# Kernel tuning notes

Measured on AMD Instinct MI355X. Metric: run time of the kernel, lower is better.

## Reference

```python
import jax, jax.numpy as jnp
import numpy as np

N = 50000    # nodes
E = 800000   # edges per block
D = 128      # embed_dim
H = 8        # heads
DH = D // H  # head dim
L = 2        # layers / blocks
IN = 128     # in_feats
P = 8192     # pos/neg pairs
FF = 2 * D   # FFN hidden
NEG_SLOPE = 0.2


def layer_norm(x, g, b, eps=1e-5):
    m = x.mean(-1, keepdims=True)
    v = ((x - m) ** 2).mean(-1, keepdims=True)
    return (x - m) / jnp.sqrt(v + eps) * g + b


def setup_inputs() -> dict:
    key = jax.random.key(0)
    ks = jax.random.split(key, 32)
    f32 = jnp.float32
    def w(k, shape, fan_in):
        return jax.random.normal(k, shape, f32) * (1.0 / np.sqrt(fan_in))
    inp = {
        'x': jax.random.normal(ks[0], (N, IN), f32),
        'src': jax.random.randint(ks[1], (L, E), 0, N),
        'dst': jax.random.randint(ks[2], (L, E), 0, N),
        'pos_src': jax.random.randint(ks[3], (P,), 0, N),
        'pos_dst': jax.random.randint(ks[4], (P,), 0, N),
        'neg_src': jax.random.randint(ks[5], (P,), 0, N),
        'neg_dst': jax.random.randint(ks[6], (P,), 0, N),
        # input projection
        'W_in': w(ks[7], (IN, D), IN), 'b_in': jnp.zeros((D,), f32),
        # per-layer attention weights, stacked over L
        'Wq': w(ks[8], (L, D, D), D), 'bq': jnp.zeros((L, D), f32),
        'Wk': w(ks[9], (L, D, D), D), 'bk': jnp.zeros((L, D), f32),
        'Wv': w(ks[10], (L, D, D), D), 'bv': jnp.zeros((L, D), f32),
        'Wo': w(ks[11], (L, D, D), D), 'bo': jnp.zeros((L, D), f32),
        'ln1_g': jnp.ones((L, D), f32), 'ln1_b': jnp.zeros((L, D), f32),
        'Wf1': w(ks[12], (L, D, FF), D), 'bf1': jnp.zeros((L, FF), f32),
        'Wf2': w(ks[13], (L, FF, D), FF), 'bf2': jnp.zeros((L, D), f32),
        'ln2_g': jnp.ones((L, D), f32), 'ln2_b': jnp.zeros((L, D), f32),
        # predictor MLP: D -> D//2 -> 1
        'Wp1': w(ks[14], (D, D // 2), D), 'bp1': jnp.zeros((D // 2,), f32),
        'Wp2': w(ks[15], (D // 2, 1), D // 2), 'bp2': jnp.zeros((1,), f32),
    }
    return inp


def reference(x, src, dst, pos_src, pos_dst, neg_src, neg_dst,
              W_in, b_in, Wq, bq, Wk, bk, Wv, bv, Wo, bo,
              ln1_g, ln1_b, Wf1, bf1, Wf2, bf2, ln2_g, ln2_b,
              Wp1, bp1, Wp2, bp2):
    scale = 1.0 / np.sqrt(DH)
    h = x @ W_in + b_in  # [N, D] (dropout is identity in eval mode)
    for l in range(L):
        s_l, d_l = src[l], dst[l]
        q = (h @ Wq[l] + bq[l]).reshape(N, H, DH)
        k = (h @ Wk[l] + bk[l]).reshape(N, H, DH)
        v = (h @ Wv[l] + bv[l]).reshape(N, H, DH)
        # per-edge attention scores [E, H]
        sc = jnp.einsum('ehd,ehd->eh', q[d_l], k[s_l]) * scale
        # segment softmax over incoming edges of each dst node
        m = jax.ops.segment_max(sc, d_l, num_segments=N)   # [N, H]
        ex = jnp.exp(sc - m[d_l])
        den = jax.ops.segment_sum(ex, d_l, num_segments=N)  # [N, H]
        alpha = ex / (den[d_l] + 1e-9)
        agg = jax.ops.segment_sum(alpha[..., None] * v[s_l], d_l,
                                  num_segments=N).reshape(N, D)
        h = layer_norm(h + agg @ Wo[l] + bo[l], ln1_g[l], ln1_b[l])
        ff = jax.nn.relu(h @ Wf1[l] + bf1[l]) @ Wf2[l] + bf2[l]
        h = layer_norm(h + ff, ln2_g[l], ln2_b[l])

    def predict(a, b):
        z = h[a] * h[b]  # gather-multiply edge scoring
        z = jax.nn.leaky_relu(z @ Wp1 + bp1, NEG_SLOPE)
        return z @ Wp2 + bp2  # [P, 1]

    pos_score = predict(pos_src, pos_dst)
    neg_score = predict(neg_src, neg_dst)
    return (pos_score, neg_score, h)
```

## Files before the change

kernel.cpp:

```cpp
#include <hip/hip_runtime.h>
#include <hip/hip_bf16.h>
#include <math.h>

#define N_NODES 50000
#define NE      800000
#define D       128
#define H       8
#define DH      16
#define NLAYER  2
#define IN_F    128
#define PP      8192
#define FF      256
#define MPAD    50048
#define CAP     96
#define NBIN    196
#define BCAP    48
#define GCAP    4608
#define CHUNK   2048

typedef short  bf16x8 __attribute__((ext_vector_type(8)));
typedef float  f32x4  __attribute__((ext_vector_type(4)));
typedef __hip_bfloat16 bf16;
typedef unsigned short u16;
typedef unsigned int   u32;

__device__ __forceinline__ float bflo(u32 u) { return __uint_as_float(u << 16); }
__device__ __forceinline__ float bfhi(u32 u) { return __uint_as_float(u & 0xffff0000u); }
__device__ __forceinline__ u16 bfbits(float f) { bf16 t = __float2bfloat16(f); return *(u16*)&t; }

__global__ __launch_bounds__(256) void bin_kernel(
    const int* __restrict__ dst, const int* __restrict__ src,
    u32* __restrict__ gbin, int* __restrict__ gbin_cnt)
{
    __shared__ u32 ent[NBIN * BCAP];
    __shared__ int bcnt[NBIN];
    const int t = threadIdx.x, l = blockIdx.y;
    const int base = blockIdx.x * CHUNK;
    if (t < NBIN) bcnt[t] = 0;
    __syncthreads();
    #pragma unroll
    for (int j = 0; j < CHUNK / 256; j++) {
        int e = base + j * 256 + t;
        if (e < NE) {
            int d = dst[(size_t)l * NE + e];
            int s = src[(size_t)l * NE + e];
            int bin = d >> 8;
            int slot = atomicAdd(&bcnt[bin], 1);
            if (slot < BCAP) ent[bin * BCAP + slot] = ((u32)s << 16) | (u32)(d & 255);
        }
    }
    __syncthreads();
    if (t < NBIN) {
        int c = bcnt[t]; if (c > BCAP) c = BCAP;
        if (c > 0) {
            int gb = atomicAdd(&gbin_cnt[l * NBIN + t], c);
            u32* gp = gbin + ((size_t)l * NBIN + t) * GCAP;
            for (int i = 0; i < c; i++)
                if (gb + i < GCAP) gp[gb + i] = ent[t * BCAP + i];
        }
    }
}

__global__ __launch_bounds__(256) void expand_kernel(
    const u32* __restrict__ gbin, const int* __restrict__ gbin_cnt,
    int* __restrict__ cnt, u16* __restrict__ ssrc)
{
    __shared__ int lcnt[256];
    const int t = threadIdx.x, b = blockIdx.x, l = blockIdx.y;
    lcnt[t] = 0;
    __syncthreads();
    int n = gbin_cnt[l * NBIN + b]; if (n > GCAP) n = GCAP;
    const u32* gp = gbin + ((size_t)l * NBIN + b) * GCAP;
    for (int i = t; i < n; i += 256) {
        u32 u = gp[i];
        int dl = (int)(u & 255);
        int pos = atomicAdd(&lcnt[dl], 1);
        if (pos < CAP) {
            int d = (b << 8) + dl;
            ssrc[((size_t)l * N_NODES + d) * CAP + pos] = (u16)(u >> 16);
        }
    }
    __syncthreads();
    int d = (b << 8) + t;
    if (d < N_NODES) cnt[l * N_NODES + d] = lcnt[t];
}

__global__ void prep_kernel(const float* __restrict__ W_in,
                            const float* __restrict__ Wq, const float* __restrict__ Wk,
                            const float* __restrict__ Wv, const float* __restrict__ Wo,
                            const float* __restrict__ Wf1, const float* __restrict__ Wf2,
                            const float* __restrict__ bq, const float* __restrict__ bk,
                            const float* __restrict__ bv,
                            bf16* __restrict__ win_t, bf16* __restrict__ wqkv_t,
                            bf16* __restrict__ wo_t, bf16* __restrict__ wf1_t,
                            bf16* __restrict__ wf2_t, float* __restrict__ bqkv,
                            int* __restrict__ gbin_cnt)
{
    int id = blockIdx.x * blockDim.x + threadIdx.x;
    if (id < 16384) {
        int n = id >> 7, k = id & 127;
        win_t[id] = __float2bfloat16(W_in[k * 128 + n]);
        return;
    }
    id -= 16384;
    if (id < NLAYER * 49152) {
        int l = id / 49152, j = id % 49152;
        int r = j >> 7, k = j & 127;
        const float* Ws; int col;
        if (r < 128) { Ws = Wq; col = r; }
        else {
            int u = r - 128, hh = u >> 5, w = u & 31;
            if (w < 16) { Ws = Wk; col = hh * 16 + w; }
            else        { Ws = Wv; col = hh * 16 + w - 16; }
        }
        wqkv_t[(size_t)l * 49152 + j] = __float2bfloat16(Ws[(size_t)l * 16384 + k * 128 + col]);
        return;
    }
    id -= NLAYER * 49152;
    if (id < NLAYER * 16384) {
        int l = id / 16384, j = id % 16384;
        int n = j >> 7, k = j & 127;
        wo_t[id] = __float2bfloat16(Wo[(size_t)l * 16384 + k * 128 + n]);
        return;
    }
    id -= NLAYER * 16384;
    if (id < NLAYER * 32768) {
        int l = id / 32768, j = id % 32768;
        int n = j >> 7, k = j & 127;
        wf1_t[id] = __float2bfloat16(Wf1[(size_t)l * 32768 + k * 256 + n]);
        return;
    }
    id -= NLAYER * 32768;
    if (id < NLAYER * 32768) {
        int l = id / 32768, j = id % 32768;
        int n = j >> 8, k = j & 255;
        wf2_t[id] = __float2bfloat16(Wf2[(size_t)l * 32768 + k * 128 + n]);
        return;
    }
    id -= NLAYER * 32768;
    if (id < NLAYER * 384) {
        int l = id / 384, r = id % 384;
        float v;
        if (r < 128) v = bq[l * 128 + r];
        else {
            int u = r - 128, hh = u >> 5, w = u & 31;
            v = (w < 16) ? bk[l * 128 + hh * 16 + w] : bv[l * 128 + hh * 16 + w - 16];
        }
        bqkv[l * 384 + r] = v;
        return;
    }
    id -= NLAYER * 384;
    if (id < 2 * NBIN) gbin_cnt[id] = 0;
}

__global__ __launch_bounds__(256) void gemm_in(
    const float* __restrict__ x, const bf16* __restrict__ Wt,
    const float* __restrict__ bias,
    float* __restrict__ Cf, bf16* __restrict__ Cb)
{
    __shared__ float4 As4[1024];
    __shared__ float4 Bs4[1024];
    char* As = (char*)As4;
    char* Bs = (char*)Bs4;
    const int t = threadIdx.x;
    const int wave = t >> 6, lane = t & 63;
    const int wr = wave >> 1, wc = wave & 1;
    const int r0 = blockIdx.x * 128, c0 = blockIdx.y * 128;

    f32x4 acc[4][4] = {};

    const int lrow   = t >> 3;
    const int lcol16 = (t & 7) * 16;

    for (int k0 = 0; k0 < 128; k0 += 64) {
        #pragma unroll
        for (int p = 0; p < 4; p++) {
            int row = p * 32 + lrow;
            int grow = r0 + row;
            float4 a0 = make_float4(0.f, 0.f, 0.f, 0.f), a1 = a0;
            if (grow < N_NODES) {
                const float* ap = x + (size_t)grow * 128 + k0 + (t & 7) * 8;
                a0 = *(const float4*)(ap);
                a1 = *(const float4*)(ap + 4);
            }
            u32 w0 = ((u32)bfbits(a0.y) << 16) | bfbits(a0.x);
            u32 w1 = ((u32)bfbits(a0.w) << 16) | bfbits(a0.z);
            u32 w2 = ((u32)bfbits(a1.y) << 16) | bfbits(a1.x);
            u32 w3 = ((u32)bfbits(a1.w) << 16) | bfbits(a1.z);
            float4 bv = *(const float4*)((const char*)(Wt + (size_t)(c0 + row) * 128 + k0) + lcol16);
            int sw = lcol16 ^ ((row & 7) << 4);
            *(uint4*)(As + row * 128 + sw) = make_uint4(w0, w1, w2, w3);
            *(float4*)(Bs + row * 128 + sw) = bv;
        }
        __syncthreads();
        #pragma unroll
        for (int kk = 0; kk < 2; kk++) {
            bf16x8 af[4], bfr[4];
            int kbyte = kk * 64 + (lane >> 4) * 16;
            #pragma unroll
            for (int m = 0; m < 4; m++) {
                int rowa = wr * 64 + m * 16 + (lane & 15);
                af[m]  = *(const bf16x8*)(As + rowa * 128 + (kbyte ^ ((rowa & 7) << 4)));
                int rowb = wc * 64 + m * 16 + (lane & 15);
                bfr[m] = *(const bf16x8*)(Bs + rowb * 128 + (kbyte ^ ((rowb & 7) << 4)));
            }
            #pragma unroll
            for (int m = 0; m < 4; m++)
                #pragma unroll
                for (int n = 0; n < 4; n++)
                    acc[m][n] = __builtin_amdgcn_mfma_f32_16x16x32_bf16(af[m], bfr[n], acc[m][n], 0, 0, 0);
        }
        __syncthreads();
    }

    const int colbase = c0 + wc * 64 + (lane & 15);
    const int rowbase = r0 + wr * 64 + ((lane >> 4) << 2);
    #pragma unroll
    for (int n = 0; n < 4; n++) {
        int col = colbase + n * 16;
        float bsv = bias[col];
        #pragma unroll
        for (int m = 0; m < 4; m++) {
            #pragma unroll
            for (int i = 0; i < 4; i++) {
                int row = rowbase + m * 16 + i;
                if (row < N_NODES) {
                    float v = acc[m][n][i] + bsv;
                    Cf[(size_t)row * 128 + col] = v;
                    Cb[(size_t)row * 128 + col] = __float2bfloat16(v);
                }
            }
        }
    }
}

__global__ __launch_bounds__(256) void gemm_mfma(
    const bf16* __restrict__ A, const bf16* __restrict__ Wt,
    const float* __restrict__ bias,
    float* __restrict__ Cf, bf16* __restrict__ Cb,
    int Mvalid, int K, int Nc, int lda, int relu)
{
    __shared__ float4 As4[1024];
    __shared__ float4 Bs4[1024];
    char* As = (char*)As4;
    char* Bs = (char*)Bs4;
    const int t = threadIdx.x;
    const int wave = t >> 6, lane = t & 63;
    const int wr = wave >> 1, wc = wave & 1;
    const int r0 = blockIdx.x * 128, c0 = blockIdx.y * 128;

    f32x4 acc[4][4] = {};

    const int lrow   = t >> 3;
    const int lcol16 = (t & 7) * 16;

    for (int k0 = 0; k0 < K; k0 += 64) {
        #pragma unroll
        for (int p = 0; p < 4; p++) {
            int row = p * 32 + lrow;
            float4 av = *(const float4*)((const char*)(A  + (size_t)(r0 + row) * lda + k0) + lcol16);
            float4 bv = *(const float4*)((const char*)(Wt + (size_t)(c0 + row) * K + k0) + lcol16);
            int sw = lcol16 ^ ((row & 7) << 4);
            *(float4*)(As + row * 128 + sw) = av;
            *(float4*)(Bs + row * 128 + sw) = bv;
        }
        __syncthreads();
        #pragma unroll
        for (int kk = 0; kk < 2; kk++) {
            bf16x8 af[4], bfr[4];
            int kbyte = kk * 64 + (lane >> 4) * 16;
            #pragma unroll
            for (int m = 0; m < 4; m++) {
                int rowa = wr * 64 + m * 16 + (lane & 15);
                af[m]  = *(const bf16x8*)(As + rowa * 128 + (kbyte ^ ((rowa & 7) << 4)));
                int rowb = wc * 64 + m * 16 + (lane & 15);
                bfr[m] = *(const bf16x8*)(Bs + rowb * 128 + (kbyte ^ ((rowb & 7) << 4)));
            }
            #pragma unroll
            for (int m = 0; m < 4; m++)
                #pragma unroll
                for (int n = 0; n < 4; n++)
                    acc[m][n] = __builtin_amdgcn_mfma_f32_16x16x32_bf16(af[m], bfr[n], acc[m][n], 0, 0, 0);
        }
        __syncthreads();
    }

    const int colbase = c0 + wc * 64 + (lane & 15);
    const int rowbase = r0 + wr * 64 + ((lane >> 4) << 2);
    #pragma unroll
    for (int n = 0; n < 4; n++) {
        int col = colbase + n * 16;
        float bsv = bias[col];
        #pragma unroll
        for (int m = 0; m < 4; m++) {
            #pragma unroll
            for (int i = 0; i < 4; i++) {
                int row = rowbase + m * 16 + i;
                if (row < Mvalid) {
                    float v = acc[m][n][i] + bsv;
                    if (relu) v = fmaxf(v, 0.f);
                    if (Cf) Cf[(size_t)row * Nc + col] = v;
                    if (Cb) Cb[(size_t)row * Nc + col] = __float2bfloat16(v);
                }
            }
        }
    }
}

__global__ __launch_bounds__(256) void tail_fused(
    const bf16* __restrict__ qkv,
    const bf16* __restrict__ wo_t,
    const float* __restrict__ bo,
    const float* __restrict__ g1, const float* __restrict__ be1,
    const bf16* __restrict__ Wf1t,
    const float* __restrict__ b1,
    const bf16* __restrict__ Wf2t,
    const float* __restrict__ b2,
    const float* __restrict__ g2, const float* __restrict__ be2,
    float* __restrict__ h, bf16* __restrict__ hb)
{
    __shared__ char lds[49152];
    char* AsA = lds;
    char* Ah1 = lds;
    char* Xs  = lds + 16384;
    char* Bs  = lds + 32768;
    const int t = threadIdx.x;
    const int w = t >> 6, lane = t & 63;
    const int r0 = blockIdx.x * 64;
    const int c = lane & 15, sub = lane >> 4;

    f32x4 acc0[8] = {};
    #pragma unroll
    for (int k0 = 0; k0 < 128; k0 += 64) {
        {
            int row = t >> 2;
            int c16 = (t & 3) * 32;
            const char* ap = (const char*)(qkv + (size_t)(r0 + row) * 384 + k0);
            float4 a0 = *(const float4*)(ap + c16);
            float4 a1 = *(const float4*)(ap + c16 + 16);
            *(float4*)(AsA + row * 128 + ((c16)      ^ ((row & 7) << 4))) = a0;
            *(float4*)(AsA + row * 128 + ((c16 + 16) ^ ((row & 7) << 4))) = a1;
        }
        {
            int row = t >> 1;
            int c16 = (t & 1) * 64;
            const char* bp = (const char*)(wo_t + (size_t)row * 128 + k0);
            #pragma unroll
            for (int j = 0; j < 4; j++) {
                float4 b = *(const float4*)(bp + c16 + j * 16);
                *(float4*)(Bs + row * 128 + ((c16 + j * 16) ^ ((row & 7) << 4))) = b;
            }
        }
        __syncthreads();
        #pragma unroll
        for (int kk = 0; kk < 2; kk++) {
            int kbyte = kk * 64 + sub * 16;
            int rowa = w * 16 + c;
            bf16x8 af = *(const bf16x8*)(AsA + rowa * 128 + (kbyte ^ ((rowa & 7) << 4)));
            #pragma unroll
            for (int n = 0; n < 8; n++) {
                int rowb = n * 16 + c;
                bf16x8 bf8 = *(const bf16x8*)(Bs + rowb * 128 + (kbyte ^ ((rowb & 7) << 4)));
                acc0[n] = __builtin_amdgcn_mfma_f32_16x16x32_bf16(af, bf8, acc0[n], 0, 0, 0);
            }
        }
        __syncthreads();
    }

    float h1v[8][4];
    {
        float bsv[8], gv[8], bev[8];
        #pragma unroll
        for (int n = 0; n < 8; n++) {
            int col = n * 16 + c;
            bsv[n] = bo[col]; gv[n] = g1[col]; bev[n] = be1[col];
        }
        #pragma unroll
        for (int i = 0; i < 4; i++) {
            int row = r0 + w * 16 + sub * 4 + i;
            bool ok = row < N_NODES;
            float x[8];
            float s = 0.f;
            #pragma unroll
            for (int n = 0; n < 8; n++) {
                float res = ok ? h[(size_t)row * D + n * 16 + c] : 0.f;
                x[n] = res + acc0[n][i] + bsv[n];
                s += x[n];
            }
            s += __shfl_xor(s, 1); s += __shfl_xor(s, 2);
            s += __shfl_xor(s, 4); s += __shfl_xor(s, 8);
            float mean = s * (1.f / 128.f);
            float v = 0.f;
            #pragma unroll
            for (int n = 0; n < 8; n++) { float dd = x[n] - mean; v += dd * dd; }
            v += __shfl_xor(v, 1); v += __shfl_xor(v, 2);
            v += __shfl_xor(v, 4); v += __shfl_xor(v, 8);
            float rstd = rsqrtf(v * (1.f / 128.f) + 1e-5f);
            int lrow = w * 16 + sub * 4 + i;
            #pragma unroll
            for (int n = 0; n < 8; n++) {
                float o = (x[n] - mean) * rstd * gv[n] + bev[n];
                h1v[n][i] = o;
                int byte = (n * 16 + c) * 2;
                int addr = lrow * 256 + ((byte & ~15) ^ ((lrow & 7) << 4)) + (byte & 15);
                *(u16*)(Ah1 + addr) = bfbits(o);
            }
        }
    }
    __syncthreads();

    f32x4 acc2[8] = {};
    #pragma unroll
    for (int xh = 0; xh < 2; xh++) {
        f32x4 acc1[8] = {};
        #pragma unroll
        for (int kc = 0; kc < 2; kc++) {
            {
                int row = t >> 1;
                int off = (t & 1) * 64;
                const char* bp = (const char*)Wf1t + (size_t)(xh * 128 + row) * 256 + kc * 128 + off;
                #pragma unroll
                for (int j = 0; j < 4; j++) {
                    float4 v = *(const float4*)(bp + j * 16);
                    *(float4*)(Bs + row * 128 + ((off + j * 16) ^ ((row & 7) << 4))) = v;
                }
            }
            __syncthreads();
            #pragma unroll
            for (int kkl = 0; kkl < 2; kkl++) {
                int abyte = (kc * 2 + kkl) * 64 + sub * 16;
                int rowa = w * 16 + c;
                bf16x8 af = *(const bf16x8*)(Ah1 + rowa * 256 + (abyte ^ ((rowa & 7) << 4)));
                int bbyte = kkl * 64 + sub * 16;
                #pragma unroll
                for (int n = 0; n < 8; n++) {
                    int rowb = n * 16 + c;
                    bf16x8 bf8 = *(const bf16x8*)(Bs + rowb * 128 + (bbyte ^ ((rowb & 7) << 4)));
                    acc1[n] = __builtin_amdgcn_mfma_f32_16x16x32_bf16(af, bf8, acc1[n], 0, 0, 0);
                }
            }
            __syncthreads();
        }
        #pragma unroll
        for (int n = 0; n < 8; n++) {
            float bs = b1[xh * 128 + n * 16 + c];
            #pragma unroll
            for (int i = 0; i < 4; i++) {
                int row = w * 16 + sub * 4 + i;
                float v = fmaxf(acc1[n][i] + bs, 0.f);
                int byte = (n * 16 + c) * 2;
                int addr = row * 256 + ((byte & ~15) ^ ((row & 7) << 4)) + (byte & 15);
                *(u16*)(Xs + addr) = bfbits(v);
            }
        }
        __syncthreads();
        #pragma unroll
        for (int oh = 0; oh < 2; oh++) {
            {
                int row = t >> 2;
                int off = (t & 3) * 64;
                const char* bp = (const char*)Wf2t + (size_t)(oh * 64 + row) * 512 + xh * 256 + off;
                #pragma unroll
                for (int j = 0; j < 4; j++) {
                    float4 v = *(const float4*)(bp + j * 16);
                    *(float4*)(Bs + row * 256 + ((off + j * 16) ^ ((row & 7) << 4))) = v;
                }
            }
            __syncthreads();
            #pragma unroll
            for (int kkl = 0; kkl < 4; kkl++) {
                int xbyte = kkl * 64 + sub * 16;
                int rowa = w * 16 + c;
                bf16x8 af = *(const bf16x8*)(Xs + rowa * 256 + (xbyte ^ ((rowa & 7) << 4)));
                #pragma unroll
                for (int n = 0; n < 4; n++) {
                    int rowb = n * 16 + c;
                    bf16x8 bf8 = *(const bf16x8*)(Bs + rowb * 256 + (xbyte ^ ((rowb & 7) << 4)));
                    acc2[oh * 4 + n] = __builtin_amdgcn_mfma_f32_16x16x32_bf16(af, bf8, acc2[oh * 4 + n], 0, 0, 0);
                }
            }
            __syncthreads();
        }
    }

    {
        float bsv[8], gv[8], bev[8];
        #pragma unroll
        for (int n = 0; n < 8; n++) {
            int col = n * 16 + c;
            bsv[n] = b2[col]; gv[n] = g2[col]; bev[n] = be2[col];
        }
        #pragma unroll
        for (int i = 0; i < 4; i++) {
            int row = r0 + w * 16 + sub * 4 + i;
            bool ok = row < N_NODES;
            float x[8];
            float s = 0.f;
            #pragma unroll
            for (int n = 0; n < 8; n++) {
                x[n] = h1v[n][i] + acc2[n][i] + bsv[n];
                s += x[n];
            }
            s += __shfl_xor(s, 1); s += __shfl_xor(s, 2);
            s += __shfl_xor(s, 4); s += __shfl_xor(s, 8);
            float mean = s * (1.f / 128.f);
            float v = 0.f;
            #pragma unroll
            for (int n = 0; n < 8; n++) { float dd = x[n] - mean; v += dd * dd; }
            v += __shfl_xor(v, 1); v += __shfl_xor(v, 2);
            v += __shfl_xor(v, 4); v += __shfl_xor(v, 8);
            float rstd = rsqrtf(v * (1.f / 128.f) + 1e-5f);
            if (ok) {
                #pragma unroll
                for (int n = 0; n < 8; n++) {
                    float o = (x[n] - mean) * rstd * gv[n] + bev[n];
                    h [(size_t)row * D + n * 16 + c] = o;
                    hb[(size_t)row * D + n * 16 + c] = __float2bfloat16(o);
                }
            }
        }
    }
}

__global__ __launch_bounds__(256) void attn_fused(
    const bf16* __restrict__ qkv,
    const int* __restrict__ cnt, const u16* __restrict__ ssrc,
    bf16* __restrict__ aggout)
{
    const float S2 = 0.25f * 1.44269504088896f;
    int wid = threadIdx.x >> 6, lane = threadIdx.x & 63;
    int d = blockIdx.x * 4 + wid;
    if (d >= N_NODES) return;
    int slot = lane >> 3, h = lane & 7;

    const u32* qr = (const u32*)(qkv + (size_t)d * 384 + h * DH);
    float qf[16];
    {
        uint4 q0 = *(const uint4*)(qr);
        uint4 q1 = *(const uint4*)(qr + 4);
        qf[0]=bflo(q0.x); qf[1]=bfhi(q0.x); qf[2]=bflo(q0.y); qf[3]=bfhi(q0.y);
        qf[4]=bflo(q0.z); qf[5]=bfhi(q0.z); qf[6]=bflo(q0.w); qf[7]=bfhi(q0.w);
        qf[8]=bflo(q1.x); qf[9]=bfhi(q1.x); qf[10]=bflo(q1.y); qf[11]=bfhi(q1.y);
        qf[12]=bflo(q1.z); qf[13]=bfhi(q1.z); qf[14]=bflo(q1.w); qf[15]=bfhi(q1.w);
    }

    int deg = cnt[d];
    if (deg > CAP) deg = CAP;
    const u16* bp = ssrc + (size_t)d * CAP;
    float m2 = -INFINITY, den = 0.f;
    float acc[16] = {};

    for (int i = slot; i < deg; i += 8) {
        int s = bp[i];
        const uint4* kvp = (const uint4*)(qkv + (size_t)s * 384 + 128 + h * 32);
        uint4 k0 = kvp[0], k1 = kvp[1], v0 = kvp[2], v1 = kvp[3];
        float p = qf[0]*bflo(k0.x) + qf[1]*bfhi(k0.x)
                + qf[2]*bflo(k0.y) + qf[3]*bfhi(k0.y)
                + qf[4]*bflo(k0.z) + qf[5]*bfhi(k0.z)
                + qf[6]*bflo(k0.w) + qf[7]*bfhi(k0.w)
                + qf[8]*bflo(k1.x) + qf[9]*bfhi(k1.x)
                + qf[10]*bflo(k1.y) + qf[11]*bfhi(k1.y)
                + qf[12]*bflo(k1.z) + qf[13]*bfhi(k1.z)
                + qf[14]*bflo(k1.w) + qf[15]*bfhi(k1.w);
        float p2 = p * S2;
        float w;
        if (p2 > m2 + 8.f) {
            float f = exp2f(m2 - p2);
            den *= f;
            #pragma unroll
            for (int j = 0; j < 16; j++) acc[j] *= f;
            m2 = p2;
            w = 1.f;
        } else {
            w = exp2f(p2 - m2);
        }
        den += w;
        acc[0]  += w*bflo(v0.x); acc[1]  += w*bfhi(v0.x);
        acc[2]  += w*bflo(v0.y); acc[3]  += w*bfhi(v0.y);
        acc[4]  += w*bflo(v0.z); acc[5]  += w*bfhi(v0.z);
        acc[6]  += w*bflo(v0.w); acc[7]  += w*bfhi(v0.w);
        acc[8]  += w*bflo(v1.x); acc[9]  += w*bfhi(v1.x);
        acc[10] += w*bflo(v1.y); acc[11] += w*bfhi(v1.y);
        acc[12] += w*bflo(v1.z); acc[13] += w*bfhi(v1.z);
        acc[14] += w*bflo(v1.w); acc[15] += w*bfhi(v1.w);
    }

    #pragma unroll
    for (int o = 8; o < 64; o <<= 1) {
        float om   = __shfl_xor(m2, o);
        float oden = __shfl_xor(den, o);
        float M = fmaxf(m2, om);
        float fa = (m2 > -INFINITY) ? exp2f(m2 - M) : 0.f;
        float fb = (om > -INFINITY) ? exp2f(om - M) : 0.f;
        den = den * fa + oden * fb;
        #pragma unroll
        for (int j = 0; j < 16; j++) {
            float oa = __shfl_xor(acc[j], o);
            acc[j] = acc[j] * fa + oa * fb;
        }
        m2 = M;
    }

    float r = 1.f / (den + 1e-9f);
    float o0 = 0.f, o1 = 0.f;
    #pragma unroll
    for (int j = 0; j < 8; j++) {
        if (slot == j) { o0 = acc[2 * j]; o1 = acc[2 * j + 1]; }
    }
    bf16* op = aggout + (size_t)d * 384 + h * DH + slot * 2;
    op[0] = __float2bfloat16(o0 * r);
    op[1] = __float2bfloat16(o1 * r);
}

__global__ void predict_kernel(const float* __restrict__ h,
                               const int* __restrict__ ps, const int* __restrict__ pd,
                               const int* __restrict__ ns, const int* __restrict__ nd,
                               const float* __restrict__ Wp1, const float* __restrict__ bp1,
                               const float* __restrict__ Wp2, const float* __restrict__ bp2,
                               float* __restrict__ out)
{
    __shared__ float z[128];
    int p = blockIdx.x;
    int a, b;
    if (p < PP) { a = ps[p]; b = pd[p]; }
    else        { a = ns[p - PP]; b = nd[p - PP]; }
    int t = threadIdx.x;
    z[t]      = h[(size_t)a * D + t]      * h[(size_t)b * D + t];
    z[t + 64] = h[(size_t)a * D + t + 64] * h[(size_t)b * D + t + 64];
    __syncthreads();
    float acc = bp1[t];
    #pragma unroll 4
    for (int i = 0; i < 128; i++) acc += z[i] * Wp1[(size_t)i * 64 + t];
    acc = acc > 0.f ? acc : 0.2f * acc;
    float part = acc * Wp2[t];
    #pragma unroll
    for (int o = 32; o > 0; o >>= 1) part += __shfl_down(part, o);
    if (t == 0) out[p] = part + bp2[0];
}

extern "C" void kernel_launch(void* const* d_in, const int* in_sizes, int n_in,
                              void* d_out, int out_size, void* d_ws, size_t ws_size,
                              hipStream_t stream)
{
    const float* x       = (const float*)d_in[0];
    const int*   src     = (const int*)d_in[1];
    const int*   dst     = (const int*)d_in[2];
    const int*   pos_src = (const int*)d_in[3];
    const int*   pos_dst = (const int*)d_in[4];
    const int*   neg_src = (const int*)d_in[5];
    const int*   neg_dst = (const int*)d_in[6];
    const float* W_in = (const float*)d_in[7];
    const float* b_in = (const float*)d_in[8];
    const float* Wq = (const float*)d_in[9];
    const float* bq = (const float*)d_in[10];
    const float* Wk = (const float*)d_in[11];
    const float* bk = (const float*)d_in[12];
    const float* Wv = (const float*)d_in[13];
    const float* bv = (const float*)d_in[14];
    const float* Wo = (const float*)d_in[15];
    const float* bo = (const float*)d_in[16];
    const float* ln1g = (const float*)d_in[17];
    const float* ln1b = (const float*)d_in[18];
    const float* Wf1 = (const float*)d_in[19];
    const float* bf1 = (const float*)d_in[20];
    const float* Wf2 = (const float*)d_in[21];
    const float* bf2 = (const float*)d_in[22];
    const float* ln2g = (const float*)d_in[23];
    const float* ln2b = (const float*)d_in[24];
    const float* Wp1 = (const float*)d_in[25];
    const float* bp1 = (const float*)d_in[26];
    const float* Wp2 = (const float*)d_in[27];
    const float* bp2 = (const float*)d_in[28];

    float* out = (float*)d_out;
    float* h   = out + 2 * PP;

    bf16* B    = (bf16*)d_ws;
    bf16* qkvb = B;
    bf16* hb   = B + (size_t)MPAD * 384;
    int*  cnt  = (int*)(hb + (size_t)MPAD * 128);
    u16*  ssrc = (u16*)(cnt + 2 * N_NODES);
    bf16* wtb  = (bf16*)(ssrc + (size_t)2 * N_NODES * CAP);
    bf16* win_t  = wtb;
    bf16* wqkv_t = wtb + 16384;
    bf16* wo_t   = wtb + 16384 + 98304;
    bf16* wf1_t  = wtb + 16384 + 98304 + 32768;
    bf16* wf2_t  = wtb + 16384 + 98304 + 32768 + 65536;
    float* bqkv  = (float*)(wtb + 16384 + 98304 + 32768 + 65536 + 65536);
    int*  gbin_cnt = (int*)(bqkv + NLAYER * 384);
    u32*  gbin     = (u32*)(gbin_cnt + 2 * NBIN);

    auto cdiv = [](int a, int b) { return (a + b - 1) / b; };
    const int GX = MPAD / 128;
    const int GL = MPAD / 64;

    prep_kernel<<<1093, 256, 0, stream>>>(W_in, Wq, Wk, Wv, Wo, Wf1, Wf2, bq, bk, bv,
                                          win_t, wqkv_t, wo_t, wf1_t, wf2_t, bqkv, gbin_cnt);
    bin_kernel<<<dim3(cdiv(NE, CHUNK), 2), 256, 0, stream>>>(dst, src, gbin, gbin_cnt);
    expand_kernel<<<dim3(NBIN, 2), 256, 0, stream>>>(gbin, gbin_cnt, cnt, ssrc);

    gemm_in<<<dim3(GX, 1), 256, 0, stream>>>(x, win_t, b_in, h, hb);

    for (int l = 0; l < NLAYER; l++) {
        gemm_mfma<<<dim3(GX, 3), 256, 0, stream>>>(hb, wqkv_t + l * 49152, bqkv + l * 384,
                                                   nullptr, qkvb, N_NODES, 128, 384, 128, 0);

        attn_fused<<<cdiv(N_NODES, 4), 256, 0, stream>>>(qkvb, cnt + l * N_NODES,
                                                         ssrc + (size_t)l * N_NODES * CAP, qkvb);

        tail_fused<<<GL, 256, 0, stream>>>(qkvb, wo_t + l * 16384, bo + l * D,
                                           ln1g + l * D, ln1b + l * D,
                                           wf1_t + l * 32768, bf1 + l * FF,
                                           wf2_t + l * 32768, bf2 + l * D,
                                           ln2g + l * D, ln2b + l * D, h, hb);
    }

    predict_kernel<<<2 * PP, 64, 0, stream>>>(h, pos_src, pos_dst, neg_src, neg_dst,
                                              Wp1, bp1, Wp2, bp2, out);
}
```

Measured before the change: 340.3 us.

## Split QKV buffer into separate Q and packed KV arrays; batch predictor pairs per block

The QKV GEMM now writes Q into a 128-wide buffer and K/V into a separate 256-wide buffer. Each gathered neighbour row in attention therefore comes from a compact KV array with a 512-byte stride instead of 768 bytes, which should give better cache and TLB locality on the edge gathers. The attention output overwrites Q in place and feeds the tail kernel. The predictor now runs 512 blocks of 256 threads. Each block stages Wp1 in LDS once and scores 32 pairs, replacing the global weight reads in every one of 16384 tiny blocks, at the cost of 32KB of LDS and extra barriers.

```diff
diff --git a/kernel.cpp b/kernel.cpp
--- a/kernel.cpp
+++ b/kernel.cpp
@@ -234,11 +234,10 @@
     }
 }
 
-__global__ __launch_bounds__(256) void gemm_mfma(
+__global__ __launch_bounds__(256) void gemm_qkv(
     const bf16* __restrict__ A, const bf16* __restrict__ Wt,
     const float* __restrict__ bias,
-    float* __restrict__ Cf, bf16* __restrict__ Cb,
-    int Mvalid, int K, int Nc, int lda, int relu)
+    bf16* __restrict__ qb, bf16* __restrict__ kvb)
 {
     __shared__ float4 As4[1024];
     __shared__ float4 Bs4[1024];
@@ -254,12 +253,12 @@
     const int lrow   = t >> 3;
     const int lcol16 = (t & 7) * 16;
 
-    for (int k0 = 0; k0 < K; k0 += 64) {
+    for (int k0 = 0; k0 < 128; k0 += 64) {
         #pragma unroll
         for (int p = 0; p < 4; p++) {
             int row = p * 32 + lrow;
-            float4 av = *(const float4*)((const char*)(A  + (size_t)(r0 + row) * lda + k0) + lcol16);
-            float4 bv = *(const float4*)((const char*)(Wt + (size_t)(c0 + row) * K + k0) + lcol16);
+            float4 av = *(const float4*)((const char*)(A  + (size_t)(r0 + row) * 128 + k0) + lcol16);
+            float4 bv = *(const float4*)((const char*)(Wt + (size_t)(c0 + row) * 128 + k0) + lcol16);
             int sw = lcol16 ^ ((row & 7) << 4);
             *(float4*)(As + row * 128 + sw) = av;
             *(float4*)(Bs + row * 128 + sw) = bv;
@@ -296,11 +295,10 @@
             #pragma unroll
             for (int i = 0; i < 4; i++) {
                 int row = rowbase + m * 16 + i;
-                if (row < Mvalid) {
+                if (row < N_NODES) {
                     float v = acc[m][n][i] + bsv;
-                    if (relu) v = fmaxf(v, 0.f);
-                    if (Cf) Cf[(size_t)row * Nc + col] = v;
-                    if (Cb) Cb[(size_t)row * Nc + col] = __float2bfloat16(v);
+                    if (col < 128) qb [(size_t)row * 128 + col]         = __float2bfloat16(v);
+                    else           kvb[(size_t)row * 256 + (col - 128)] = __float2bfloat16(v);
                 }
             }
         }
@@ -308,7 +306,7 @@
 }
 
 __global__ __launch_bounds__(256) void tail_fused(
-    const bf16* __restrict__ qkv,
+    const bf16* __restrict__ qb,
     const bf16* __restrict__ wo_t,
     const float* __restrict__ bo,
     const float* __restrict__ g1, const float* __restrict__ be1,
@@ -335,7 +333,7 @@
         {
             int row = t >> 2;
             int c16 = (t & 3) * 32;
-            const char* ap = (const char*)(qkv + (size_t)(r0 + row) * 384 + k0);
+            const char* ap = (const char*)(qb + (size_t)(r0 + row) * 128 + k0);
             float4 a0 = *(const float4*)(ap + c16);
             float4 a1 = *(const float4*)(ap + c16 + 16);
             *(float4*)(AsA + row * 128 + ((c16)      ^ ((row & 7) << 4))) = a0;
@@ -523,7 +521,7 @@
 }
 
 __global__ __launch_bounds__(256) void attn_fused(
-    const bf16* __restrict__ qkv,
+    const bf16* __restrict__ qb, const bf16* __restrict__ kvb,
     const int* __restrict__ cnt, const u16* __restrict__ ssrc,
     bf16* __restrict__ aggout)
 {
@@ -533,7 +531,7 @@
     if (d >= N_NODES) return;
     int slot = lane >> 3, h = lane & 7;
 
-    const u32* qr = (const u32*)(qkv + (size_t)d * 384 + h * DH);
+    const u32* qr = (const u32*)(qb + (size_t)d * 128 + h * DH);
     float qf[16];
     {
         uint4 q0 = *(const uint4*)(qr);
@@ -552,7 +550,7 @@
 
     for (int i = slot; i < deg; i += 8) {
         int s = bp[i];
-        const uint4* kvp = (const uint4*)(qkv + (size_t)s * 384 + 128 + h * 32);
+        const uint4* kvp = (const uint4*)(kvb + (size_t)s * 256 + h * 32);
         uint4 k0 = kvp[0], k1 = kvp[1], v0 = kvp[2], v1 = kvp[3];
         float p = qf[0]*bflo(k0.x) + qf[1]*bfhi(k0.x)
                 + qf[2]*bflo(k0.y) + qf[3]*bfhi(k0.y)
@@ -607,35 +605,47 @@
     for (int j = 0; j < 8; j++) {
         if (slot == j) { o0 = acc[2 * j]; o1 = acc[2 * j + 1]; }
     }
-    bf16* op = aggout + (size_t)d * 384 + h * DH + slot * 2;
+    bf16* op = aggout + (size_t)d * 128 + h * DH + slot * 2;
     op[0] = __float2bfloat16(o0 * r);
     op[1] = __float2bfloat16(o1 * r);
 }
 
-__global__ void predict_kernel(const float* __restrict__ h,
-                               const int* __restrict__ ps, const int* __restrict__ pd,
-                               const int* __restrict__ ns, const int* __restrict__ nd,
-                               const float* __restrict__ Wp1, const float* __restrict__ bp1,
-                               const float* __restrict__ Wp2, const float* __restrict__ bp2,
-                               float* __restrict__ out)
-{
-    __shared__ float z[128];
-    int p = blockIdx.x;
-    int a, b;
-    if (p < PP) { a = ps[p]; b = pd[p]; }
-    else        { a = ns[p - PP]; b = nd[p - PP]; }
-    int t = threadIdx.x;
-    z[t]      = h[(size_t)a * D + t]      * h[(size_t)b * D + t];
-    z[t + 64] = h[(size_t)a * D + t + 64] * h[(size_t)b * D + t + 64];
+__global__ __launch_bounds__(256) void predict_kernel(
+    const float* __restrict__ h,
+    const int* __restrict__ ps, const int* __restrict__ pd,
+    const int* __restrict__ ns, const int* __restrict__ nd,
+    const float* __restrict__ Wp1, const float* __restrict__ bp1,
+    const float* __restrict__ Wp2, const float* __restrict__ bp2,
+    float* __restrict__ out)
+{
+    __shared__ float Wp1s[8192];
+    __shared__ float bp1s[64], wp2s[64];
+    __shared__ float zbuf[4][128];
+    const int t = threadIdx.x;
+    const int wv = t >> 6, lane = t & 63;
+    for (int j = t; j < 8192; j += 256) Wp1s[j] = Wp1[j];
+    if (t < 64) { bp1s[t] = bp1[t]; wp2s[t] = Wp2[t]; }
     __syncthreads();
-    float acc = bp1[t];
-    #pragma unroll 4
-    for (int i = 0; i < 128; i++) acc += z[i] * Wp1[(size_t)i * 64 + t];
-    acc = acc > 0.f ? acc : 0.2f * acc;
-    float part = acc * Wp2[t];
+
     #pragma unroll
-    for (int o = 32; o > 0; o >>= 1) part += __shfl_down(part, o);
-    if (t == 0) out[p] = part + bp2[0];
+    for (int it = 0; it < 8; it++) {
+        int p = blockIdx.x * 32 + wv * 8 + it;
+        int a, b;
+        if (p < PP) { a = ps[p]; b = pd[p]; }
+        else        { a = ns[p - PP]; b = nd[p - PP]; }
+        zbuf[wv][lane]      = h[(size_t)a * D + lane]      * h[(size_t)b * D + lane];
+        zbuf[wv][lane + 64] = h[(size_t)a * D + lane + 64] * h[(size_t)b * D + lane + 64];
+        __syncthreads();
+        float acc = bp1s[lane];
+        #pragma unroll 4
+        for (int i = 0; i < 128; i++) acc += zbuf[wv][i] * Wp1s[i * 64 + lane];
+        acc = acc > 0.f ? acc : 0.2f * acc;
+        float part = acc * wp2s[lane];
+        #pragma unroll
+        for (int o = 32; o > 0; o >>= 1) part += __shfl_down(part, o);
+        if (lane == 0) out[p] = part + bp2[0];
+        __syncthreads();
+    }
 }
 
 extern "C" void kernel_launch(void* const* d_in, const int* in_sizes, int n_in,
@@ -676,7 +686,8 @@
     float* h   = out + 2 * PP;
 
     bf16* B    = (bf16*)d_ws;
-    bf16* qkvb = B;
+    bf16* qb   = B;
+    bf16* kvb  = B + (size_t)MPAD * 128;
     bf16* hb   = B + (size_t)MPAD * 384;
     int*  cnt  = (int*)(hb + (size_t)MPAD * 128);
     u16*  ssrc = (u16*)(cnt + 2 * N_NODES);
@@ -702,19 +713,18 @@
     gemm_in<<<dim3(GX, 1), 256, 0, stream>>>(x, win_t, b_in, h, hb);
 
     for (int l = 0; l < NLAYER; l++) {
-        gemm_mfma<<<dim3(GX, 3), 256, 0, stream>>>(hb, wqkv_t + l * 49152, bqkv + l * 384,
-                                                   nullptr, qkvb, N_NODES, 128, 384, 128, 0);
-
-        attn_fused<<<cdiv(N_NODES, 4), 256, 0, stream>>>(qkvb, cnt + l * N_NODES,
-                                                         ssrc + (size_t)l * N_NODES * CAP, qkvb);
-
-        tail_fused<<<GL, 256, 0, stream>>>(qkvb, wo_t + l * 16384, bo + l * D,
+        gemm_qkv<<<dim3(GX, 3), 256, 0, stream>>>(hb, wqkv_t + l * 49152, bqkv + l * 384, qb, kvb);
+
+        attn_fused<<<cdiv(N_NODES, 4), 256, 0, stream>>>(qb, kvb, cnt + l * N_NODES,
+                                                         ssrc + (size_t)l * N_NODES * CAP, qb);
+
+        tail_fused<<<GL, 256, 0, stream>>>(qb, wo_t + l * 16384, bo + l * D,
                                            ln1g + l * D, ln1b + l * D,
                                            wf1_t + l * 32768, bf1 + l * FF,
                                            wf2_t + l * 32768, bf2 + l * D,
                                            ln2g + l * D, ln2b + l * D, h, hb);
     }
 
-    predict_kernel<<<2 * PP, 64, 0, stream>>>(h, pos_src, pos_dst, neg_src, neg_dst,
-                                              Wp1, bp1, Wp2, bp2, out);
-}
+    predict_kernel<<<512, 256, 0, stream>>>(h, pos_src, pos_dst, neg_src, neg_dst,
+                                            Wp1, bp1, Wp2, bp2, out);
+}
```

Measured after the change: 336.2 us. Within noise of the previous version (-1.2%).
